# Kernel optimization log

Measured on AMD Instinct MI355X. Metric: run time of the kernel, lower is better.

The kernel has to match this reference:

```python
import jax, jax.numpy as jnp
import numpy as np

B, S, H, NH = 2, 2048, 1024, 16
DH = H // NH  # 64

def setup_inputs() -> dict:
    key = jax.random.key(0)
    ks = jax.random.split(key, 6)
    return {
        "hidden_states": jax.random.normal(ks[0], (B, S, H), jnp.float32),
        "attention_mask": jnp.zeros((B, 1, 1, S), jnp.float32),  # additive mask (0 = attend)
        "local_attention_mask": jax.random.randint(ks[1], (B, 1, S, S), 0, 2).astype(jnp.int32),
        "gate_outputs": jax.random.uniform(ks[2], (B, NH, S, 1), jnp.float32),
        "Wq": jax.random.normal(ks[3], (H, H), jnp.float32) * 0.02,
        "bq": jnp.zeros((H,), jnp.float32),
        "Wk": jax.random.normal(ks[4], (H, H), jnp.float32) * 0.02,
        "bk": jnp.zeros((H,), jnp.float32),
        "Wv": jax.random.normal(ks[5], (H, H), jnp.float32) * 0.02,
        "bv": jnp.zeros((H,), jnp.float32),
    }

def _heads(x):
    # [B,S,H] -> [B,NH,S,DH]
    return x.reshape(B, S, NH, DH).transpose(0, 2, 1, 3)

def reference(hidden_states, attention_mask, local_attention_mask, gate_outputs, Wq, bq, Wk, bk, Wv, bv):
    q = _heads(hidden_states @ Wq.T + bq)
    k = _heads(hidden_states @ Wk.T + bk)
    v = _heads(hidden_states @ Wv.T + bv)
    scores = jnp.einsum("bhqd,bhkd->bhqk", q, k) / jnp.sqrt(jnp.float32(DH))
    # global branch (additive mask)
    probs_g = jax.nn.softmax(scores + attention_mask, axis=-1)
    ctx_g = jnp.einsum("bhqk,bhkd->bhqd", probs_g, v)
    # local branch: 0/1 mask -> additive -inf mask
    lmask = (1.0 - local_attention_mask.astype(jnp.float32)) * jnp.finfo(jnp.float32).min
    probs_l = jax.nn.softmax(scores + lmask, axis=-1)
    ctx_l = jnp.einsum("bhqk,bhkd->bhqd", probs_l, v)
    ctx = gate_outputs * ctx_l + (1.0 - gate_outputs) * ctx_g  # [B,NH,S,DH]
    return ctx.transpose(0, 2, 1, 3).reshape(B, S, H)
```

## Files before the change

### kernel.cpp

```cpp
#include <hip/hip_runtime.h>
#include <cstdint>
#include <cstddef>

typedef short short8 __attribute__((ext_vector_type(8)));
typedef short short4v __attribute__((ext_vector_type(4)));
typedef float floatx4 __attribute__((ext_vector_type(4)));
typedef unsigned short ushort4v __attribute__((ext_vector_type(4)));

constexpr int B_ = 2, S_ = 2048, H_ = 1024, NH_ = 16, DH_ = 64;
constexpr int K_ = H_;

__device__ __forceinline__ unsigned short f2bf(float f) {
  unsigned u = __float_as_uint(f);
  u += 0x7fffu + ((u >> 16) & 1u);
  return (unsigned short)(u >> 16);
}

__device__ __forceinline__ unsigned pack2bf(float a, float b) {
  unsigned ua = (__float_as_uint(a) + 0x8000u) >> 16;
  unsigned ub = (__float_as_uint(b) + 0x8000u) & 0xffff0000u;
  return ua | ub;
}

__global__ __launch_bounds__(256) void cvt_bf16(const float* __restrict__ in,
                                                unsigned short* __restrict__ out, int n) {
  int i = (blockIdx.x * blockDim.x + threadIdx.x) * 4;
  if (i >= n) return;
  float4 v = *reinterpret_cast<const float4*>(in + i);
  ushort4v o;
  o.x = f2bf(v.x); o.y = f2bf(v.y); o.z = f2bf(v.z); o.w = f2bf(v.w);
  *reinterpret_cast<ushort4v*>(out + i) = o;
}

__global__ __launch_bounds__(256) void build_bitmask(const int* __restrict__ lm,
                                                     unsigned long long* __restrict__ bm) {
  int word = blockIdx.x * 4 + (threadIdx.x >> 6);
  int lane = threadIdx.x & 63;
  unsigned long long bits = __ballot(lm[(size_t)word * 64 + lane] != 0);
  if (lane == 0) bm[word] = bits;
}

__global__ __launch_bounds__(256) void build_eam(const float* __restrict__ am,
                                                 float* __restrict__ ea) {
  int i = blockIdx.x * 256 + threadIdx.x;
  ea[i] = __expf(am[i]);
}

typedef __attribute__((address_space(1))) const void gvoid;
typedef __attribute__((address_space(3))) void lvoid;
__device__ __forceinline__ void async16(const unsigned short* gp, unsigned short* lp) {
  __builtin_amdgcn_global_load_lds((gvoid*)gp, (lvoid*)lp, 16, 0, 0);
}

__global__ __launch_bounds__(256) void gemm_qkv(
    const unsigned short* __restrict__ A,
    const unsigned short* __restrict__ Wq, const unsigned short* __restrict__ Wk,
    const unsigned short* __restrict__ Wv,
    const float* __restrict__ bq, const float* __restrict__ bk, const float* __restrict__ bv,
    unsigned short* __restrict__ qo, unsigned short* __restrict__ ko,
    unsigned short* __restrict__ vo) {
  __shared__ alignas(16) unsigned short As[128 * 32];
  __shared__ alignas(16) unsigned short Bs[128 * 32];
  const int z = blockIdx.z;
  const unsigned short* W = (z == 0) ? Wq : (z == 1) ? Wk : Wv;
  const float* bias = (z == 0) ? bq : (z == 1) ? bk : bv;

  const int m0 = blockIdx.x * 128, n0 = blockIdx.y * 128;
  const int tid = threadIdx.x, lane = tid & 63, wvi = tid >> 6;
  const int wr = wvi >> 1, wc = wvi & 1, quad = lane >> 4, l16 = lane & 15;

  floatx4 zf = {0.f, 0.f, 0.f, 0.f};
  floatx4 acc[4][4];
  for (int i = 0; i < 4; i++)
    for (int j = 0; j < 4; j++) acc[i][j] = zf;

  for (int kk = 0; kk < K_; kk += 32) {
#pragma unroll
    for (int i = 0; i < 2; i++) {
      int cb = wvi * 128 + i * 64;
      int c = cb + lane;
      int row = c >> 2, kc = c & 3;
      async16(A + (size_t)(m0 + row) * K_ + kk + kc * 8, As + cb * 8);
      async16(W + (size_t)(n0 + row) * K_ + kk + kc * 8, Bs + cb * 8);
    }
    __syncthreads();
    short8 af[4], bfr[4];
#pragma unroll
    for (int mf = 0; mf < 4; mf++)
      af[mf] = *reinterpret_cast<const short8*>(&As[(wr * 64 + mf * 16 + l16) * 32 + quad * 8]);
#pragma unroll
    for (int nf = 0; nf < 4; nf++)
      bfr[nf] = *reinterpret_cast<const short8*>(&Bs[(wc * 64 + nf * 16 + l16) * 32 + quad * 8]);
#pragma unroll
    for (int mf = 0; mf < 4; mf++)
#pragma unroll
      for (int nf = 0; nf < 4; nf++)
        acc[mf][nf] = __builtin_amdgcn_mfma_f32_16x16x32_bf16(af[mf], bfr[nf], acc[mf][nf], 0, 0, 0);
    __syncthreads();
  }

  unsigned short* outp = (z == 0) ? qo : (z == 1) ? ko : vo;
#pragma unroll
  for (int mf = 0; mf < 4; mf++) {
    int mbase = m0 + wr * 64 + mf * 16 + quad * 4;
    int b = mbase >> 11, s0 = mbase & 2047;
#pragma unroll
    for (int nf = 0; nf < 4; nf++) {
      int n = n0 + wc * 64 + nf * 16 + l16;
      int h = n >> 6, d = n & 63;
      int bh = b * NH_ + h;
      float bvv = bias[n];
      floatx4 c = acc[mf][nf];
      if (z == 0) {
#pragma unroll
        for (int r = 0; r < 4; r++) {
          float val = (c[r] + bvv) * 0.125f;
          outp[((size_t)bh * S_ + (s0 + r)) * DH_ + d] = f2bf(val);
        }
      } else if (z == 1) {
        size_t base = (size_t)bh * 131072 + (s0 >> 6) * 4096 + ((s0 >> 4) & 3) * 1024 +
                      (d >> 5) * 512 + ((d >> 3) & 3) * 128 + (d & 7);
#pragma unroll
        for (int r = 0; r < 4; r++)
          outp[base + ((s0 & 15) + r) * 8] = f2bf(c[r] + bvv);
      } else {
        size_t base = (size_t)bh * 131072 + (s0 >> 6) * 4096 + (d >> 4) * 1024 +
                      ((s0 >> 4) & 3) * 256 + ((s0 >> 2) & 3) * 64 + (d & 15) * 4;
        ushort4v p;
        p.x = f2bf(c[0] + bvv); p.y = f2bf(c[1] + bvv);
        p.z = f2bf(c[2] + bvv); p.w = f2bf(c[3] + bvv);
        *reinterpret_cast<ushort4v*>(&outp[base]) = p;
      }
    }
  }
}

__global__ __launch_bounds__(256, 4) void attn_kernel(
    const unsigned short* __restrict__ q,
    const unsigned short* __restrict__ kperm,
    const unsigned short* __restrict__ vperm,
    const float* __restrict__ eam,
    const unsigned long long* __restrict__ bm,
    const float* __restrict__ gate,
    float* __restrict__ out) {
  __shared__ alignas(16) unsigned short Ks[2][4096];
  __shared__ alignas(16) unsigned short Vs[2][4096];

  const int flat = blockIdx.x;
  const int h = (flat & 7) + 8 * ((flat >> 3) & 1);
  const int b = (flat >> 4) & 1;
  const int qt = flat >> 5;
  const int tid = threadIdx.x, lane = tid & 63, wvi = tid >> 6;
  const int quad = lane >> 4, l16 = lane & 15;
  const int bh = b * NH_ + h;
  const int q0 = qt * 64 + wvi * 16;

  const unsigned short* qrow = q + ((size_t)bh * S_ + q0 + l16) * DH_;
  short8 qf0 = *reinterpret_cast<const short8*>(qrow + quad * 8);
  short8 qf1 = *reinterpret_cast<const short8*>(qrow + 32 + quad * 8);

  floatx4 zf = {0.f, 0.f, 0.f, 0.f};
  float psg = 0.f, psl = 0.f;
  floatx4 accg[4], accl[4];
#pragma unroll
  for (int i = 0; i < 4; i++) { accg[i] = zf; accl[i] = zf; }

  const unsigned short* kp = kperm + (size_t)bh * 131072;
  const unsigned short* vp = vperm + (size_t)bh * 131072;
  const float* eamb = eam + (size_t)b * S_;
  const unsigned long long* bmq = bm + ((size_t)b * S_ + q0 + l16) * (S_ / 64);

  const unsigned short* kg0 = kp + tid * 16;
  const unsigned short* vg0 = vp + tid * 16;
  const int so = tid * 16;

  uint4 pk0 = *reinterpret_cast<const uint4*>(kg0);
  uint4 pk1 = *reinterpret_cast<const uint4*>(kg0 + 8);
  uint4 pv0 = *reinterpret_cast<const uint4*>(vg0);
  uint4 pv1 = *reinterpret_cast<const uint4*>(vg0 + 8);
  *reinterpret_cast<uint4*>(&Ks[0][so]) = pk0;
  *reinterpret_cast<uint4*>(&Ks[0][so + 8]) = pk1;
  *reinterpret_cast<uint4*>(&Vs[0][so]) = pv0;
  *reinterpret_cast<uint4*>(&Vs[0][so + 8]) = pv1;

  for (int kt = 0; kt < S_ / 64; kt++) {
    __syncthreads();
    {
      const int tb = ((kt + 1) & 31) * 4096;
      pk0 = *reinterpret_cast<const uint4*>(kg0 + tb);
      pk1 = *reinterpret_cast<const uint4*>(kg0 + tb + 8);
      pv0 = *reinterpret_cast<const uint4*>(vg0 + tb);
      pv1 = *reinterpret_cast<const uint4*>(vg0 + tb + 8);
    }
    const int k0 = kt * 64;
    unsigned long long w = bmq[kt];
    float4 ea[4];
#pragma unroll
    for (int t = 0; t < 4; t++)
      ea[t] = *reinterpret_cast<const float4*>(eamb + k0 + t * 16 + quad * 4);

    const unsigned short* Kc = Ks[kt & 1];
    const unsigned short* Vc = Vs[kt & 1];
    floatx4 scT[4];
#pragma unroll
    for (int t = 0; t < 4; t++) {
      const unsigned short* kr = Kc + t * 1024 + lane * 8;
      short8 kf0 = *reinterpret_cast<const short8*>(kr);
      short8 kf1 = *reinterpret_cast<const short8*>(kr + 512);
      scT[t] = __builtin_amdgcn_mfma_f32_16x16x32_bf16(kf0, qf0, zf, 0, 0, 0);
      scT[t] = __builtin_amdgcn_mfma_f32_16x16x32_bf16(kf1, qf1, scT[t], 0, 0, 0);
    }
    int pgf[4][2], plf[4][2];
#pragma unroll
    for (int t = 0; t < 4; t++) {
      unsigned m4 = (unsigned)(w >> (t * 16 + quad * 4)) & 0xFu;
      float e0 = __expf(scT[t][0]), e1 = __expf(scT[t][1]);
      float e2 = __expf(scT[t][2]), e3 = __expf(scT[t][3]);
      float g0 = e0 * ea[t].x, g1 = e1 * ea[t].y, g2 = e2 * ea[t].z, g3 = e3 * ea[t].w;
      psg += (g0 + g1) + (g2 + g3);
      float l0 = (m4 & 1u) ? e0 : 0.f;
      float l1 = (m4 & 2u) ? e1 : 0.f;
      float l2 = (m4 & 4u) ? e2 : 0.f;
      float l3 = (m4 & 8u) ? e3 : 0.f;
      psl += (l0 + l1) + (l2 + l3);
      pgf[t][0] = pack2bf(g0, g1); pgf[t][1] = pack2bf(g2, g3);
      plf[t][0] = pack2bf(l0, l1); plf[t][1] = pack2bf(l2, l3);
    }
#pragma unroll
    for (int d = 0; d < 4; d++) {
#pragma unroll
      for (int t = 0; t < 4; t++) {
        short4v vf = *reinterpret_cast<const short4v*>(Vc + d * 1024 + t * 256 + lane * 4);
        short4v pg = *reinterpret_cast<const short4v*>(&pgf[t][0]);
        short4v pl = *reinterpret_cast<const short4v*>(&plf[t][0]);
        accg[d] = __builtin_amdgcn_mfma_f32_16x16x16bf16_1k(vf, pg, accg[d], 0, 0, 0);
        accl[d] = __builtin_amdgcn_mfma_f32_16x16x16bf16_1k(vf, pl, accl[d], 0, 0, 0);
      }
    }
    __syncthreads();
    {
      const int bn = (kt + 1) & 1;
      *reinterpret_cast<uint4*>(&Ks[bn][so]) = pk0;
      *reinterpret_cast<uint4*>(&Ks[bn][so + 8]) = pk1;
      *reinterpret_cast<uint4*>(&Vs[bn][so]) = pv0;
      *reinterpret_cast<uint4*>(&Vs[bn][so + 8]) = pv1;
    }
  }

  float lgf = psg;
  lgf += __shfl_xor(lgf, 16, 64);
  lgf += __shfl_xor(lgf, 32, 64);
  float llf = psl;
  llf += __shfl_xor(llf, 16, 64);
  llf += __shfl_xor(llf, 32, 64);
  const int s = q0 + l16;
  const float g = gate[(size_t)bh * S_ + s];
  const float cg = (1.f - g) / lgf, cl = g / llf;
  float* orow = out + ((size_t)b * S_ + s) * H_ + h * DH_ + quad * 4;
#pragma unroll
  for (int d = 0; d < 4; d++) {
    float4 o;
    o.x = cl * accl[d][0] + cg * accg[d][0];
    o.y = cl * accl[d][1] + cg * accg[d][1];
    o.z = cl * accl[d][2] + cg * accg[d][2];
    o.w = cl * accl[d][3] + cg * accg[d][3];
    *reinterpret_cast<float4*>(orow + d * 16) = o;
  }
}

extern "C" void kernel_launch(void* const* d_in, const int* in_sizes, int n_in,
                              void* d_out, int out_size, void* d_ws, size_t ws_size,
                              hipStream_t stream) {
  (void)in_sizes; (void)n_in; (void)out_size; (void)ws_size;
  const float* hs = (const float*)d_in[0];
  const float* am = (const float*)d_in[1];
  const int* lm = (const int*)d_in[2];
  const float* gate = (const float*)d_in[3];
  const float* Wq = (const float*)d_in[4];
  const float* bq = (const float*)d_in[5];
  const float* Wk = (const float*)d_in[6];
  const float* bk = (const float*)d_in[7];
  const float* Wv = (const float*)d_in[8];
  const float* bv = (const float*)d_in[9];
  float* out = (float*)d_out;

  unsigned short* ws = (unsigned short*)d_ws;
  unsigned short* hbf = ws;
  unsigned short* wqb = hbf + 4194304;
  unsigned short* wkb = wqb + 1048576;
  unsigned short* wvb = wkb + 1048576;
  unsigned short* qb = wvb + 1048576;
  unsigned short* kb = qb + 4194304;
  unsigned short* vtb = kb + 4194304;
  unsigned long long* bmp = (unsigned long long*)(vtb + 4194304);
  float* eamp = (float*)(bmp + 131072);

  cvt_bf16<<<4096, 256, 0, stream>>>(hs, hbf, 4194304);
  cvt_bf16<<<1024, 256, 0, stream>>>(Wq, wqb, 1048576);
  cvt_bf16<<<1024, 256, 0, stream>>>(Wk, wkb, 1048576);
  cvt_bf16<<<1024, 256, 0, stream>>>(Wv, wvb, 1048576);
  build_bitmask<<<32768, 256, 0, stream>>>(lm, bmp);
  build_eam<<<16, 256, 0, stream>>>(am, eamp);
  gemm_qkv<<<dim3(32, 8, 3), 256, 0, stream>>>(hbf, wqb, wkb, wvb, bq, bk, bv, qb, kb, vtb);
  attn_kernel<<<dim3(1024), 256, 0, stream>>>(qb, kb, vtb, eamp, bmp, gate, out);
}
```

Baseline: 285.4 us.

## Deepen K/V prefetch, drop one barrier per tile, fold log2e into Q

The K/V staging loop now keeps global loads two tiles ahead in registers. It writes them to the alternate LDS buffer right after the single barrier at the top of each iteration, which removes the second __syncthreads per tile. Per-thread loads are split into two 8-element chunks at tid*8 and 2048+tid*8, which improves coalescing across lanes. The Q projection scale now includes log2(e), so the softmax can call the native exp2 instead of __expf and skip the per-element multiply. The tradeoffs are more registers held live across the loop and a prefetch index that wraps on the final tiles.

```diff
diff --git a/kernel.cpp b/kernel.cpp
--- a/kernel.cpp
+++ b/kernel.cpp
@@ -114,7 +114,7 @@
       if (z == 0) {
 #pragma unroll
         for (int r = 0; r < 4; r++) {
-          float val = (c[r] + bvv) * 0.125f;
+          float val = (c[r] + bvv) * 0.18033688011112042f;
           outp[((size_t)bh * S_ + (s0 + r)) * DH_ + d] = f2bf(val);
         }
       } else if (z == 1) {
@@ -170,27 +170,40 @@
   const float* eamb = eam + (size_t)b * S_;
   const unsigned long long* bmq = bm + ((size_t)b * S_ + q0 + l16) * (S_ / 64);
 
-  const unsigned short* kg0 = kp + tid * 16;
-  const unsigned short* vg0 = vp + tid * 16;
-  const int so = tid * 16;
-
-  uint4 pk0 = *reinterpret_cast<const uint4*>(kg0);
-  uint4 pk1 = *reinterpret_cast<const uint4*>(kg0 + 8);
-  uint4 pv0 = *reinterpret_cast<const uint4*>(vg0);
-  uint4 pv1 = *reinterpret_cast<const uint4*>(vg0 + 8);
-  *reinterpret_cast<uint4*>(&Ks[0][so]) = pk0;
-  *reinterpret_cast<uint4*>(&Ks[0][so + 8]) = pk1;
-  *reinterpret_cast<uint4*>(&Vs[0][so]) = pv0;
-  *reinterpret_cast<uint4*>(&Vs[0][so + 8]) = pv1;
+  const int soA = tid * 8, soB = 2048 + tid * 8;
+  const unsigned short* kgA = kp + soA;
+  const unsigned short* kgB = kp + soB;
+  const unsigned short* vgA = vp + soA;
+  const unsigned short* vgB = vp + soB;
+
+  uint4 pk0 = *reinterpret_cast<const uint4*>(kgA);
+  uint4 pk1 = *reinterpret_cast<const uint4*>(kgB);
+  uint4 pv0 = *reinterpret_cast<const uint4*>(vgA);
+  uint4 pv1 = *reinterpret_cast<const uint4*>(vgB);
+  *reinterpret_cast<uint4*>(&Ks[0][soA]) = pk0;
+  *reinterpret_cast<uint4*>(&Ks[0][soB]) = pk1;
+  *reinterpret_cast<uint4*>(&Vs[0][soA]) = pv0;
+  *reinterpret_cast<uint4*>(&Vs[0][soB]) = pv1;
+  pk0 = *reinterpret_cast<const uint4*>(kgA + 4096);
+  pk1 = *reinterpret_cast<const uint4*>(kgB + 4096);
+  pv0 = *reinterpret_cast<const uint4*>(vgA + 4096);
+  pv1 = *reinterpret_cast<const uint4*>(vgB + 4096);
 
   for (int kt = 0; kt < S_ / 64; kt++) {
     __syncthreads();
     {
-      const int tb = ((kt + 1) & 31) * 4096;
-      pk0 = *reinterpret_cast<const uint4*>(kg0 + tb);
-      pk1 = *reinterpret_cast<const uint4*>(kg0 + tb + 8);
-      pv0 = *reinterpret_cast<const uint4*>(vg0 + tb);
-      pv1 = *reinterpret_cast<const uint4*>(vg0 + tb + 8);
+      const int bn = (kt + 1) & 1;
+      *reinterpret_cast<uint4*>(&Ks[bn][soA]) = pk0;
+      *reinterpret_cast<uint4*>(&Ks[bn][soB]) = pk1;
+      *reinterpret_cast<uint4*>(&Vs[bn][soA]) = pv0;
+      *reinterpret_cast<uint4*>(&Vs[bn][soB]) = pv1;
+    }
+    {
+      const int tb = ((kt + 2) & 31) * 4096;
+      pk0 = *reinterpret_cast<const uint4*>(kgA + tb);
+      pk1 = *reinterpret_cast<const uint4*>(kgB + tb);
+      pv0 = *reinterpret_cast<const uint4*>(vgA + tb);
+      pv1 = *reinterpret_cast<const uint4*>(vgB + tb);
     }
     const int k0 = kt * 64;
     unsigned long long w = bmq[kt];
@@ -214,8 +227,10 @@
 #pragma unroll
     for (int t = 0; t < 4; t++) {
       unsigned m4 = (unsigned)(w >> (t * 16 + quad * 4)) & 0xFu;
-      float e0 = __expf(scT[t][0]), e1 = __expf(scT[t][1]);
-      float e2 = __expf(scT[t][2]), e3 = __expf(scT[t][3]);
+      float e0 = __builtin_amdgcn_exp2f(scT[t][0]);
+      float e1 = __builtin_amdgcn_exp2f(scT[t][1]);
+      float e2 = __builtin_amdgcn_exp2f(scT[t][2]);
+      float e3 = __builtin_amdgcn_exp2f(scT[t][3]);
       float g0 = e0 * ea[t].x, g1 = e1 * ea[t].y, g2 = e2 * ea[t].z, g3 = e3 * ea[t].w;
       psg += (g0 + g1) + (g2 + g3);
       float l0 = (m4 & 1u) ? e0 : 0.f;
@@ -236,14 +251,6 @@
         accg[d] = __builtin_amdgcn_mfma_f32_16x16x16bf16_1k(vf, pg, accg[d], 0, 0, 0);
         accl[d] = __builtin_amdgcn_mfma_f32_16x16x16bf16_1k(vf, pl, accl[d], 0, 0, 0);
       }
-    }
-    __syncthreads();
-    {
-      const int bn = (kt + 1) & 1;
-      *reinterpret_cast<uint4*>(&Ks[bn][so]) = pk0;
-      *reinterpret_cast<uint4*>(&Ks[bn][so + 8]) = pk1;
-      *reinterpret_cast<uint4*>(&Vs[bn][so]) = pv0;
-      *reinterpret_cast<uint4*>(&Vs[bn][so + 8]) = pv1;
     }
   }
 
```

Result: no change. 279.8 us (-2.0%).
